# Kernel tuning notes

Hardware: AMD Instinct MI355X
Metric: run time of the kernel (lower is better)

The kernel has to match this reference:

```python
import jax, jax.numpy as jnp
import numpy as np

K = 1024   # in_dim = out_dim = per-head dim (module uses full k per head)
H = 4      # heads
B, T = 2, 2048


def setup_inputs() -> dict:
    key = jax.random.key(0)
    ks = jax.random.split(key, 7)
    s = 0.02
    return {
        "x": jax.random.normal(ks[0], (B, T, K), jnp.float32),
        "Wq": jax.random.normal(ks[1], (K, K * H), jnp.float32) * s,
        "Wk": jax.random.normal(ks[2], (K, K * H), jnp.float32) * s,
        "Wv": jax.random.normal(ks[3], (K, K * H), jnp.float32) * s,
        "Wu": jax.random.normal(ks[4], (K * H, K), jnp.float32) * s,
        "bu": jnp.zeros((K,), jnp.float32),
        "W1": jax.random.normal(ks[5], (K, K), jnp.float32) * s,
        "b1": jnp.zeros((K,), jnp.float32),
        "W2": jax.random.normal(ks[6], (K, K), jnp.float32) * s,
        "b2": jnp.zeros((K,), jnp.float32),
    }


def reference(x, Wq, Wk, Wv, Wu, bu, W1, b1, W2, b2):
    b, t, k = x.shape
    h = H
    scale = k ** (-0.25)
    # projections: each head gets FULL dim k (quirk of the original module)
    q = (x @ Wq).reshape(b, t, h, k) * scale   # [b,t,h,k]
    kk = (x @ Wk).reshape(b, t, h, k) * scale
    v = (x @ Wv).reshape(b, t, h, k)
    # attention scores [b,h,q,k_pos]
    dot = jnp.einsum("bqhd,bkhd->bhqk", q, kk)
    causal = jnp.tril(jnp.ones((t, t), bool))  # strictly-upper masked to -inf
    dot = jnp.where(causal, dot, -jnp.inf)
    attn = jax.nn.softmax(dot, axis=-1)
    out = jnp.einsum("bhqk,bkhd->bqhd", attn, v).reshape(b, t, h * k)
    attn_out = out @ Wu + bu                   # unifyheads
    x = x + attn_out                            # residual
    ff = jax.nn.relu(x @ W1 + b1) @ W2 + b2     # in_dim == out_dim
    return x + ff                               # residual around FFN
```

## Files before the change

kernel.cpp:

```cpp
#include <hip/hip_runtime.h>
#include <math.h>


typedef __attribute__((ext_vector_type(8))) short short8;
typedef __attribute__((ext_vector_type(4))) float f32x4;

__device__ __forceinline__ unsigned short f2bf(float f) {
  union { float f; unsigned int u; } v; v.f = f;
  unsigned int r = (v.u + 0x7fffu + ((v.u >> 16) & 1u)) >> 16;
  return (unsigned short)r;
}
__device__ __forceinline__ float bf2f(unsigned short b) {
  union { unsigned int u; float f; } v; v.u = ((unsigned int)b) << 16;
  return v.f;
}

#define GL2LDS(g, l)                                                          \
  __builtin_amdgcn_global_load_lds(                                           \
      (__attribute__((address_space(1))) void*)(g),                           \
      (__attribute__((address_space(3))) void*)(l), 16, 0, 0)

__device__ __forceinline__ void core256(
    const unsigned short* __restrict__ A, const unsigned short* __restrict__ BT,
    int m0, int n0, int kmax, int lda, int ldb, int ldc, long long coff,
    unsigned short* __restrict__ Cb, unsigned short* lds) {
  const int tid = threadIdx.x;
  const int lane = tid & 63;
  const int wid = tid >> 6;
  const int wm = wid >> 2;
  const int wn = wid & 3;

  unsigned short* Als = lds;
  unsigned short* Bls = lds + 32768;

  const int srow = wid * 8 + (lane >> 3);
  const int scol = ((lane & 7) ^ (lane >> 3)) * 8;
  const unsigned short* ag = A + (long long)(m0 + srow) * lda + scol;
  const unsigned short* bg = BT + (long long)(n0 + srow) * ldb + scol;

  const int frow = lane & 15;
  const int lq = lane >> 4;
  const int fsw = frow & 7;

  f32x4 acc[8][4];
#pragma unroll
  for (int i = 0; i < 8; ++i)
#pragma unroll
    for (int j = 0; j < 4; ++j) acc[i][j] = {0.f, 0.f, 0.f, 0.f};

  short8 afr[4][2];
  short8 bfrE[2][2];
  short8 bfrO[2][2];

  const int NT = kmax >> 6;

  auto stageA = [&](int t_, int h_) {
    unsigned short* d = Als + (t_ & 1) * 16384 + h_ * 8192 + wid * 512;
    const unsigned short* g = ag + ((long long)h_ * 128) * lda + t_ * 64;
    GL2LDS(g, d);
    GL2LDS(g + (long long)64 * lda, d + 4096);
  };
  auto stageB = [&](int t_, int h_) {
    unsigned short* d = Bls + (t_ & 1) * 16384 + h_ * 8192 + wid * 512;
    const unsigned short* g = bg + ((long long)h_ * 128) * ldb + t_ * 64;
    GL2LDS(g, d);
    GL2LDS(g + (long long)64 * ldb, d + 4096);
  };

#define RDA(QM)                                                               \
  _Pragma("unroll")                                                           \
  for (int m_ = 0; m_ < 4; ++m_)                                              \
    _Pragma("unroll")                                                         \
    for (int kh_ = 0; kh_ < 2; ++kh_)                                         \
      afr[m_][kh_] = *(const short8*)(Als + b * 16384 + wm * 8192 +           \
          ((QM) * 64 + m_ * 16 + frow) * 64 + ((kh_ * 4 + lq) ^ fsw) * 8);

#define RDB(QN, BFR)                                                          \
  _Pragma("unroll")                                                           \
  for (int n_ = 0; n_ < 2; ++n_)                                              \
    _Pragma("unroll")                                                         \
    for (int kh_ = 0; kh_ < 2; ++kh_)                                         \
      BFR[n_][kh_] = *(const short8*)(Bls + b * 16384 + (wn >> 1) * 8192 +    \
          ((wn & 1) * 64 + (QN) * 32 + n_ * 16 + frow) * 64 +                 \
          ((kh_ * 4 + lq) ^ fsw) * 8);

#define QUAD(QM, QN, BFR)                                                     \
  do {                                                                        \
    __builtin_amdgcn_s_setprio(1);                                            \
    _Pragma("unroll")                                                         \
    for (int m_ = 0; m_ < 4; ++m_)                                            \
      _Pragma("unroll")                                                       \
      for (int n_ = 0; n_ < 2; ++n_)                                          \
        _Pragma("unroll")                                                     \
        for (int kh_ = 0; kh_ < 2; ++kh_)                                     \
          acc[(QM) * 4 + m_][(QN) * 2 + n_] =                                 \
              __builtin_amdgcn_mfma_f32_16x16x32_bf16(                        \
                  afr[m_][kh_], BFR[n_][kh_],                                 \
                  acc[(QM) * 4 + m_][(QN) * 2 + n_], 0, 0, 0);                \
    __builtin_amdgcn_s_setprio(0);                                            \
  } while (0)

  stageA(0, 0); stageA(0, 1); stageB(0, 0); stageB(0, 1);

  for (int t = 0; t < NT; ++t) {
    const int b = t & 1;
    const bool pf = (t + 1 < NT);
    if (pf) {
      stageA(t + 1, 0); stageA(t + 1, 1);
      asm volatile("s_waitcnt vmcnt(4)" ::: "memory");
    } else {
      asm volatile("s_waitcnt vmcnt(0)" ::: "memory");
    }
    __builtin_amdgcn_s_barrier();
    RDA(0)
    RDB(0, bfrE)
    asm volatile("s_waitcnt lgkmcnt(0)" ::: "memory");
    __builtin_amdgcn_sched_barrier(0);
    QUAD(0, 0, bfrE);
    __builtin_amdgcn_sched_barrier(0);
    __builtin_amdgcn_s_barrier();
    RDB(1, bfrO)
    if (pf) { stageB(t + 1, 0); stageB(t + 1, 1); }
    __builtin_amdgcn_s_barrier();
    asm volatile("s_waitcnt lgkmcnt(0)" ::: "memory");
    __builtin_amdgcn_sched_barrier(0);
    QUAD(0, 1, bfrO);
    __builtin_amdgcn_sched_barrier(0);
    __builtin_amdgcn_s_barrier();
    RDA(1)
    __builtin_amdgcn_s_barrier();
    asm volatile("s_waitcnt lgkmcnt(0)" ::: "memory");
    __builtin_amdgcn_sched_barrier(0);
    QUAD(1, 1, bfrO);
    __builtin_amdgcn_sched_barrier(0);
    __builtin_amdgcn_s_barrier();
    QUAD(1, 0, bfrE);
    __builtin_amdgcn_sched_barrier(0);
  }
#undef RDA
#undef RDB
#undef QUAD

  const int ccol = lane & 15;
  const int crow = lq * 4;
#pragma unroll
  for (int mi = 0; mi < 8; ++mi) {
#pragma unroll
    for (int ni = 0; ni < 4; ++ni) {
      const int gc = n0 + wn * 64 + ni * 16 + ccol;
#pragma unroll
      for (int r = 0; r < 4; ++r) {
        const int gr = m0 + wm * 128 + mi * 16 + crow + r;
        Cb[coff + (long long)gr * ldc + gc] = f2bf(acc[mi][ni][r]);
      }
    }
  }
}


__global__ __launch_bounds__(512, 2) void g256_cmb(
    const unsigned short* __restrict__ Wkc,
    const unsigned short* __restrict__ Wqc,
    unsigned short* __restrict__ Wcomb) {
  __shared__ unsigned short lds[65536];
  const long long Mi = 1024 * 1024;
  const int bid = blockIdx.x;
  const int z = bid & 7, zb = z >> 2, zh = z & 3;
  const int j = bid >> 3;
  const int m0 = (j & 3) * 256, n0 = (j >> 2) * 256;
  core256(Wkc + (long long)zb * 4 * Mi + zh * 1024,
          Wqc + (long long)zb * 4 * Mi + zh * 1024,
          m0, n0, 1024, 4096, 4096, 1024,
          (long long)zb * 4 * Mi + (long long)zh * Mi, Wcomb, lds);
}

__global__ __launch_bounds__(512, 2) void g256_t(
    const unsigned short* __restrict__ xb,
    const unsigned short* __restrict__ Wcomb,
    unsigned short* __restrict__ tb) {
  __shared__ unsigned short lds[65536];
  const int bid = blockIdx.x;
  const int xcd = bid & 7;
  const int j = bid >> 3;
  const int m0 = (xcd * 2 + (j & 1)) * 256;
  const int n0 = (j >> 1) * 256;
  core256(xb, Wcomb, m0, n0, 1024, 1024, 1024, 4096, 0, tb, lds);
}

__global__ __launch_bounds__(512, 2) void g256_sv(
    const unsigned short* __restrict__ xb,
    const unsigned short* __restrict__ Wcomb,
    const unsigned short* __restrict__ tb,
    unsigned short* __restrict__ S, unsigned short* __restrict__ vT) {
  __shared__ unsigned short lds[65536];
  const long long TT = (long long)2048 * 2048;
  const int bid = blockIdx.x;
  if (bid < 288) {
    const int z = bid & 7, zb = z >> 2, zh = z & 3;
    const int idx = bid >> 3;
    int m = (int)((sqrtf(8.0f * idx + 1.0f) - 1.0f) * 0.5f);
    while ((m + 1) * (m + 2) / 2 <= idx) ++m;
    while (m * (m + 1) / 2 > idx) --m;
    const int m0 = m * 256;
    const int n0 = (idx - m * (m + 1) / 2) * 256;
    core256(tb + (long long)zb * 2048 * 4096 + zh * 1024,
            xb + (long long)zb * 2048 * 1024,
            m0, n0, 1024, 4096, 1024, 2048,
            (long long)(zb * 4 + zh) * TT, S, lds);
  } else {
    const int r = bid - 288;
    const int xcd = r & 7;
    const int j = r >> 3;
    const int m0 = (xcd * 2 + (j & 1)) * 256;
    const int rest = j >> 1;
    const int bb = rest >> 3;
    const int n0 = (rest & 7) * 256;
    core256(Wcomb + (size_t)4096 * 1024, xb + (long long)bb * 2048 * 1024,
            m0, n0, 1024, 1024, 1024, 2048, (long long)bb * 4096 * 2048,
            vT, lds);
  }
}

__global__ __launch_bounds__(512, 2) void g256_pv(
    const unsigned short* __restrict__ S, const unsigned short* __restrict__ vT,
    unsigned short* __restrict__ Pb) {
  __shared__ unsigned short lds[65536];
  const long long TT = (long long)2048 * 2048;
  const long long MN = (long long)4096 * 1024;
  const int z = blockIdx.x, zb = z >> 2, zh = z & 3;
  const int m0 = blockIdx.y * 256, n0 = blockIdx.z * 256;
  core256(S + (long long)(zb * 4 + zh) * TT,
          vT + (long long)zb * 4096 * 2048 + (long long)zh * 1024 * 2048,
          m0, n0, m0 + 256, 2048, 2048, 1024,
          (long long)zh * MN + (long long)zb * 2048 * 1024, Pb, lds);
}

__device__ __forceinline__ void core64(
    f32x4 acc[4][2], const unsigned short* __restrict__ A, int lda,
    const unsigned short* __restrict__ BT, int ldb, int kmax,
    unsigned short* As, unsigned short* Bs) {
  const int tid = threadIdx.x;
  const int lane = tid & 63;
  const int wv = tid >> 6;
  const int wm = wv & 1;
  const int wn = wv >> 1;
  const int srow = tid >> 2;
  const int scol = (((tid & 3) ^ ((srow >> 1) & 3)) * 8);
  const unsigned short* ap0 = A + (long long)srow * lda + scol;
  const unsigned short* ap1 = ap0 + (long long)64 * lda;
  const unsigned short* bp0 = BT + (long long)srow * ldb + scol;
  unsigned short* lA = As + wv * 512;
  unsigned short* lB = Bs + wv * 512;
  const int frow = lane & 15;
  const int fqs = (((lane >> 4) ^ ((frow >> 1) & 3)) * 8);

  int rs = 0, rc = 0;

  auto stage = [&]() {
    unsigned short* a = lA + rs * 4096;
    GL2LDS(ap0, a); GL2LDS(ap1, a + 2048);
    GL2LDS(bp0, lB + rs * 2048);
    ap0 += 32; ap1 += 32; bp0 += 32;
    rs ^= 1;
  };
  auto compute = [&]() {
    const unsigned short* Ac = As + rc * 4096;
    const unsigned short* Bc = Bs + rc * 2048;
    short8 afr[4], bfr[2];
#pragma unroll
    for (int mi = 0; mi < 4; ++mi)
      afr[mi] = *(const short8*)(Ac + (wm * 64 + mi * 16 + frow) * 32 + fqs);
#pragma unroll
    for (int ni = 0; ni < 2; ++ni)
      bfr[ni] = *(const short8*)(Bc + (wn * 32 + ni * 16 + frow) * 32 + fqs);
    __builtin_amdgcn_s_setprio(1);
#pragma unroll
    for (int mi = 0; mi < 4; ++mi)
#pragma unroll
      for (int ni = 0; ni < 2; ++ni)
        acc[mi][ni] = __builtin_amdgcn_mfma_f32_16x16x32_bf16(
            afr[mi], bfr[ni], acc[mi][ni], 0, 0, 0);
    __builtin_amdgcn_s_setprio(0);
    rc ^= 1;
  };

  const int nsteps = kmax >> 5;
  stage();
  for (int i = 0; i + 1 < nsteps; ++i) {
    stage();
    asm volatile("s_waitcnt vmcnt(3)" ::: "memory");
    __builtin_amdgcn_s_barrier();
    __builtin_amdgcn_sched_barrier(0);
    compute();
    __builtin_amdgcn_sched_barrier(0);
    __builtin_amdgcn_s_barrier();
  }
  asm volatile("s_waitcnt vmcnt(0)" ::: "memory");
  __builtin_amdgcn_s_barrier();
  __builtin_amdgcn_sched_barrier(0);
  compute();
}

__global__ __launch_bounds__(256) void gemm_ffn(
    const unsigned short* __restrict__ A, const unsigned short* __restrict__ BT,
    const float* __restrict__ bias, const float* __restrict__ resid,
    int do_relu, float* __restrict__ Cf, unsigned short* __restrict__ Cb) {
  __shared__ unsigned short As[8192];
  __shared__ unsigned short Bs[4096];
  const int bid = blockIdx.x;
  const int xcd = bid & 7;
  const int j = bid >> 3;
  const int m0 = (xcd * 4 + (j & 3)) * 128;
  const int n0 = (j >> 2) * 64;
  f32x4 acc[4][2];
#pragma unroll
  for (int i = 0; i < 4; ++i)
#pragma unroll
    for (int j2 = 0; j2 < 2; ++j2) acc[i][j2] = {0.f, 0.f, 0.f, 0.f};
  core64(acc, A + (long long)m0 * 1024, 1024, BT + (long long)n0 * 1024, 1024,
         1024, As, Bs);
  const int lane = threadIdx.x & 63;
  const int wv = threadIdx.x >> 6;
  const int wm = wv & 1, wn = wv >> 1;
  const int ccol = lane & 15, crow = (lane >> 4) * 4;
#pragma unroll
  for (int mi = 0; mi < 4; ++mi) {
#pragma unroll
    for (int ni = 0; ni < 2; ++ni) {
      const int gc = n0 + wn * 32 + ni * 16 + ccol;
#pragma unroll
      for (int r = 0; r < 4; ++r) {
        const int gr = m0 + wm * 64 + mi * 16 + crow + r;
        float v = acc[mi][ni][r] + bias[gc];
        if (resid) v += resid[(long long)gr * 1024 + gc];
        if (do_relu) v = fmaxf(v, 0.f);
        const long long ci = (long long)gr * 1024 + gc;
        if (Cf) Cf[ci] = v;
        if (Cb) Cb[ci] = f2bf(v);
      }
    }
  }
}

__global__ __launch_bounds__(256) void reduce_epi(
    const unsigned short* __restrict__ Pb, int S, long long MN,
    const float* __restrict__ bias, const float* __restrict__ resid,
    int do_relu, float* __restrict__ Cf, unsigned short* __restrict__ Cb) {
  const long long i4 = ((long long)blockIdx.x * 256 + threadIdx.x) * 4;
  if (i4 >= MN) return;
  float4 s = {0.f, 0.f, 0.f, 0.f};
  for (int t = 0; t < S; ++t) {
    const ushort4 p = *(const ushort4*)(Pb + (long long)t * MN + i4);
    s.x += bf2f(p.x); s.y += bf2f(p.y); s.z += bf2f(p.z); s.w += bf2f(p.w);
  }
  if (bias) {
    const int c0 = (int)(i4 & 1023);
    s.x += bias[c0]; s.y += bias[c0 + 1]; s.z += bias[c0 + 2]; s.w += bias[c0 + 3];
  }
  if (resid) {
    const float4 rr = *(const float4*)(resid + i4);
    s.x += rr.x; s.y += rr.y; s.z += rr.z; s.w += rr.w;
  }
  if (do_relu) {
    s.x = fmaxf(s.x, 0.f); s.y = fmaxf(s.y, 0.f);
    s.z = fmaxf(s.z, 0.f); s.w = fmaxf(s.w, 0.f);
  }
  if (Cf) *(float4*)(Cf + i4) = s;
  if (Cb) {
    ushort4 o;
    o.x = f2bf(s.x); o.y = f2bf(s.y); o.z = f2bf(s.z); o.w = f2bf(s.w);
    *(ushort4*)(Cb + i4) = o;
  }
}

__global__ __launch_bounds__(256) void softmax_causal(unsigned short* S, int T) {
  const int q = blockIdx.x;
  unsigned short* row = S + ((long long)blockIdx.y * T + q) * T;
  const int tid = threadIdx.x;
  const int lane = tid & 63;
  const int wv = tid >> 6;
  const int n = q + 1;
  const int nz = (n + 255) & ~255;
  const int base = tid * 8;
  short8 raw = {};
  if (base < nz) raw = *(const short8*)(row + base);
  float vals[8];
  float m = -__builtin_inff();
#pragma unroll
  for (int i = 0; i < 8; ++i) {
    vals[i] = (base + i < n) ? bf2f((unsigned short)raw[i]) : -__builtin_inff();
    m = fmaxf(m, vals[i]);
  }
#pragma unroll
  for (int o = 32; o; o >>= 1) m = fmaxf(m, __shfl_xor(m, o, 64));
  __shared__ float red[4];
  if (lane == 0) red[wv] = m;
  __syncthreads();
  m = fmaxf(fmaxf(red[0], red[1]), fmaxf(red[2], red[3]));
  __syncthreads();
  float s = 0.f, e[8];
#pragma unroll
  for (int i = 0; i < 8; ++i) {
    e[i] = (base + i < n) ? __expf(vals[i] - m) : 0.f;
    s += e[i];
  }
#pragma unroll
  for (int o = 32; o; o >>= 1) s += __shfl_xor(s, o, 64);
  if (lane == 0) red[wv] = s;
  __syncthreads();
  s = red[0] + red[1] + red[2] + red[3];
  const float inv = 1.f / s;
  if (base < nz) {
    short8 o8;
#pragma unroll
    for (int i = 0; i < 8; ++i) o8[i] = (short)f2bf(e[i] * inv);
    *(short8*)(row + base) = o8;
  }
}

__global__ __launch_bounds__(256) void prep_all(
    const float* __restrict__ x, const float* __restrict__ Wq,
    const float* __restrict__ Wk, const float* __restrict__ Wv,
    const float* __restrict__ Wu, const float* __restrict__ W1,
    const float* __restrict__ W2, unsigned short* __restrict__ xb,
    unsigned short* __restrict__ Wqc, unsigned short* __restrict__ Wkc,
    unsigned short* __restrict__ Wvc, unsigned short* __restrict__ WuTb,
    unsigned short* __restrict__ W1T, unsigned short* __restrict__ W2T,
    float s2) {
  const int z = blockIdx.y;
  if (z <= 3) {
    const float* src = (z == 0) ? x : (z == 1) ? Wq : (z == 2) ? Wk : Wv;
    unsigned short* dst = (z == 0) ? xb : (z == 1) ? Wqc : (z == 2) ? Wkc : Wvc;
    const float sc = (z == 2) ? s2 : 1.0f;
    const long long i4 = ((long long)blockIdx.x * 256 + threadIdx.x) * 4;
    const float4 v = *(const float4*)(src + i4);
    ushort4 u;
    u.x = f2bf(v.x * sc); u.y = f2bf(v.y * sc);
    u.z = f2bf(v.z * sc); u.w = f2bf(v.w * sc);
    *(ushort4*)(dst + i4) = u;
    return;
  }
  const int R = (z == 4) ? 4096 : 1024;
  const int by = blockIdx.x >> 5;
  if (by * 32 >= R) return;
  const float* W = (z == 4) ? Wu : (z == 5) ? W1 : W2;
  unsigned short* WT = (z == 4) ? WuTb : (z == 5) ? W1T : W2T;
  __shared__ float tile[32][33];
  const int c0 = (blockIdx.x & 31) * 32;
  const int r0 = by * 32;
  const int tx = threadIdx.x & 31;
  const int ty = threadIdx.x >> 5;
#pragma unroll
  for (int j = 0; j < 32; j += 8)
    tile[ty + j][tx] = W[(long long)(r0 + ty + j) * 1024 + c0 + tx];
  __syncthreads();
#pragma unroll
  for (int j = 0; j < 32; j += 8)
    WT[(long long)(c0 + ty + j) * R + r0 + tx] = f2bf(tile[tx][ty + j]);
}

extern "C" void kernel_launch(void* const* d_in, const int* in_sizes, int n_in,
                              void* d_out, int out_size, void* d_ws,
                              size_t ws_size, hipStream_t stream) {
  (void)in_sizes; (void)n_in; (void)out_size; (void)ws_size;
  const float* x  = (const float*)d_in[0];
  const float* Wq = (const float*)d_in[1];
  const float* Wk = (const float*)d_in[2];
  const float* Wv = (const float*)d_in[3];
  const float* Wu = (const float*)d_in[4];
  const float* bu = (const float*)d_in[5];
  const float* W1 = (const float*)d_in[6];
  const float* b1 = (const float*)d_in[7];
  const float* W2 = (const float*)d_in[8];
  const float* b2 = (const float*)d_in[9];
  float* out = (float*)d_out;

  const int T = 2048;
  const size_t MB = 1024 * 1024;
  const long long MN = (long long)4096 * 1024;

  char* w = (char*)d_ws;
  unsigned short* xb    = (unsigned short*)(w + 0 * MB);
  unsigned short* Wqc   = (unsigned short*)(w + 8 * MB);
  unsigned short* Wvc   = (unsigned short*)(w + 16 * MB);
  unsigned short* Wkc   = (unsigned short*)(w + 24 * MB);
  unsigned short* WuTb  = (unsigned short*)(w + 32 * MB);
  unsigned short* Wcomb = (unsigned short*)(w + 40 * MB);
  unsigned short* tb    = (unsigned short*)(w + 56 * MB);
  unsigned short* vT    = (unsigned short*)(w + 88 * MB);
  unsigned short* S     = (unsigned short*)(w + 120 * MB);
  unsigned short* W1T   = (unsigned short*)(w + 184 * MB);
  unsigned short* W2T   = (unsigned short*)(w + 186 * MB);
  unsigned short* Pb    = (unsigned short*)(w + 40 * MB);
  float*          x1f   = (float*)(w + 8 * MB);
  unsigned short* x1b   = (unsigned short*)(w + 24 * MB);
  unsigned short* h1    = (unsigned short*)(w + 32 * MB);
  (void)WuTb; (void)Wvc;

  const float s2 = 0.03125f;

  prep_all<<<dim3(4096, 7), 256, 0, stream>>>(
      x, Wq, Wk, Wv, Wu, W1, W2, xb, Wqc, Wkc, Wvc, WuTb, W1T, W2T, s2);

  g256_cmb<<<dim3(128), 512, 0, stream>>>(Wkc, Wqc, Wcomb);

  g256_t<<<dim3(256), 512, 0, stream>>>(xb, Wcomb, tb);

  g256_sv<<<dim3(544), 512, 0, stream>>>(xb, Wcomb, tb, S, vT);

  softmax_causal<<<dim3(T, 8), 256, 0, stream>>>(S, T);

  g256_pv<<<dim3(8, 8, 4), 512, 0, stream>>>(S, vT, Pb);

  reduce_epi<<<dim3(4096), 256, 0, stream>>>(Pb, 4, MN, bu, x, 0, x1f, x1b);

  gemm_ffn<<<dim3(512), 256, 0, stream>>>(x1b, W1T, b1, nullptr, 1,
                                          nullptr, h1);

  gemm_ffn<<<dim3(512), 256, 0, stream>>>(h1, W2T, b2, x1f, 0, out, nullptr);
}
```

Measured before the change: 415.9 us.

## Restructure GEMM main loop to one barrier per K-tile with fragment prefetch

Rewrites the double-buffered 256x256 GEMM inner loop. Instead of several barriers and explicit lgkmcnt waits and sched_barriers per K step, it preloads the first A/B fragments before the loop. Each iteration then issues the next tile's global-to-LDS loads, runs four MFMA quads while reading the remaining fragments, and ends with a single vmcnt wait plus barrier before reading the next buffer's first fragments. The aim is to cut synchronization stalls and let LDS reads overlap MFMA work. The risks are losing the explicit scheduling control the old code had, and possible write-after-read hazards on the buffer being refilled.

```diff
diff --git a/kernel.cpp b/kernel.cpp
--- a/kernel.cpp
+++ b/kernel.cpp
@@ -67,20 +67,20 @@
     GL2LDS(g + (long long)64 * ldb, d + 4096);
   };
 
-#define RDA(QM)                                                               \
+#define RDA(BUF, QM)                                                          \
   _Pragma("unroll")                                                           \
   for (int m_ = 0; m_ < 4; ++m_)                                              \
     _Pragma("unroll")                                                         \
     for (int kh_ = 0; kh_ < 2; ++kh_)                                         \
-      afr[m_][kh_] = *(const short8*)(Als + b * 16384 + wm * 8192 +           \
+      afr[m_][kh_] = *(const short8*)(Als + (BUF) * 16384 + wm * 8192 +       \
           ((QM) * 64 + m_ * 16 + frow) * 64 + ((kh_ * 4 + lq) ^ fsw) * 8);
 
-#define RDB(QN, BFR)                                                          \
+#define RDB(BUF, QN, BFR)                                                     \
   _Pragma("unroll")                                                           \
   for (int n_ = 0; n_ < 2; ++n_)                                              \
     _Pragma("unroll")                                                         \
     for (int kh_ = 0; kh_ < 2; ++kh_)                                         \
-      BFR[n_][kh_] = *(const short8*)(Bls + b * 16384 + (wn >> 1) * 8192 +    \
+      BFR[n_][kh_] = *(const short8*)(Bls + (BUF) * 16384 + (wn >> 1) * 8192 +\
           ((wn & 1) * 64 + (QN) * 32 + n_ * 16 + frow) * 64 +                 \
           ((kh_ * 4 + lq) ^ fsw) * 8);
 
@@ -101,41 +101,28 @@
   } while (0)
 
   stageA(0, 0); stageA(0, 1); stageB(0, 0); stageB(0, 1);
+  asm volatile("s_waitcnt vmcnt(0)" ::: "memory");
+  __builtin_amdgcn_s_barrier();
+  RDA(0, 0)
+  RDB(0, 0, bfrE)
 
   for (int t = 0; t < NT; ++t) {
     const int b = t & 1;
     const bool pf = (t + 1 < NT);
+    if (pf) { stageA(t + 1, 0); stageA(t + 1, 1); }
+    QUAD(0, 0, bfrE);
+    RDB(b, 1, bfrO)
+    if (pf) { stageB(t + 1, 0); stageB(t + 1, 1); }
+    QUAD(0, 1, bfrO);
+    RDA(b, 1)
+    QUAD(1, 0, bfrE);
+    QUAD(1, 1, bfrO);
+    asm volatile("s_waitcnt vmcnt(0)" ::: "memory");
+    __builtin_amdgcn_s_barrier();
     if (pf) {
-      stageA(t + 1, 0); stageA(t + 1, 1);
-      asm volatile("s_waitcnt vmcnt(4)" ::: "memory");
-    } else {
-      asm volatile("s_waitcnt vmcnt(0)" ::: "memory");
+      RDA(b ^ 1, 0)
+      RDB(b ^ 1, 0, bfrE)
     }
-    __builtin_amdgcn_s_barrier();
-    RDA(0)
-    RDB(0, bfrE)
-    asm volatile("s_waitcnt lgkmcnt(0)" ::: "memory");
-    __builtin_amdgcn_sched_barrier(0);
-    QUAD(0, 0, bfrE);
-    __builtin_amdgcn_sched_barrier(0);
-    __builtin_amdgcn_s_barrier();
-    RDB(1, bfrO)
-    if (pf) { stageB(t + 1, 0); stageB(t + 1, 1); }
-    __builtin_amdgcn_s_barrier();
-    asm volatile("s_waitcnt lgkmcnt(0)" ::: "memory");
-    __builtin_amdgcn_sched_barrier(0);
-    QUAD(0, 1, bfrO);
-    __builtin_amdgcn_sched_barrier(0);
-    __builtin_amdgcn_s_barrier();
-    RDA(1)
-    __builtin_amdgcn_s_barrier();
-    asm volatile("s_waitcnt lgkmcnt(0)" ::: "memory");
-    __builtin_amdgcn_sched_barrier(0);
-    QUAD(1, 1, bfrO);
-    __builtin_amdgcn_sched_barrier(0);
-    __builtin_amdgcn_s_barrier();
-    QUAD(1, 0, bfrE);
-    __builtin_amdgcn_sched_barrier(0);
   }
 #undef RDA
 #undef RDB
```

After: 403.8 us, median of 2. -2.9%, faster.
